# Performance work log

Measured on AMD Instinct MI355X. Metric: run time of the kernel, lower is better.

## Reference

```python
import jax, jax.numpy as jnp
import numpy as np

B, H, W, D = 8, 64, 64, 256   # batch, grid rows, grid cols, q_size==c_size
N = 1024                      # number of query/alignment points
R_WIN, C_WIN = 1, 2           # hardcoded window half-sizes from the module


def setup_inputs() -> dict:
    key = jax.random.key(0)
    k1, k2, k3, k4 = jax.random.split(key, 4)
    q = jax.random.normal(k1, (B, H, W, D), jnp.float32)
    c_t = jax.random.normal(k2, (B, N, D), jnp.float32)
    # float positions inside the grid: row in [0,H-1), col in [0,W-1)
    p_t = jax.random.uniform(k3, (B, N, 2), jnp.float32) * jnp.array([H - 1, W - 1], jnp.float32)
    W_a = jax.random.normal(k4, (D, D), jnp.float32) / np.sqrt(D)  # nn.Linear(q_size->c_size) weight [c,q]
    return {"q": q, "c_t": c_t, "p_t": p_t, "W_a": W_a}


def reference(q, c_t, p_t, W_a):
    Bq, Hh, Ww, Dd = q.shape
    rows, cols = Hh + 1, Ww + 1
    # ConstantPad2d((1,0,1,0), nan) on channels-first layout == pad top row & left col with NaN
    q_pad = jnp.pad(q.transpose(0, 3, 1, 2), ((0, 0), (0, 0), (1, 0), (1, 0)),
                    constant_values=jnp.nan)                      # [B,D,rows,cols]
    p0 = p_t[..., 0].astype(jnp.int32)
    p1 = p_t[..., 1].astype(jnp.int32)
    r = jnp.clip(p0[..., None] + jnp.arange(-R_WIN, R_WIN + 1) + 1, 0, rows) % rows  # [B,N,2R+1]
    c = jnp.clip(p1[..., None] + jnp.arange(-C_WIN, C_WIN + 1) + 1, 0, cols) % cols  # [B,N,2C+1]
    # flattened window indices, i (row offset) major, j (col offset) minor
    idx = (r[..., :, None] * cols + c[..., None, :]).reshape(Bq, r.shape[1], -1)     # [B,N,K]
    K = idx.shape[-1]
    q_flat = q_pad.reshape(Bq, Dd, rows * cols).transpose(0, 2, 1)                   # [B,rows*cols,D]
    qg = jnp.take_along_axis(q_flat, idx.reshape(Bq, -1, 1), axis=1)
    qg = qg.reshape(Bq, idx.shape[1], K, Dd)                                          # [B,N,K,D]
    nan_loc = jnp.isnan(qg[..., 0])                                                   # [B,N,K]
    qg = jnp.where(nan_loc[..., None], 0.0, qg)
    # Gaussian decay around the (float) predicted position
    rexp = jnp.exp(-2.0 * ((jnp.clip(r.astype(q.dtype) - 1, 0, None) - p_t[..., 0:1]) / R_WIN) ** 2)
    cexp = jnp.exp(-2.0 * ((jnp.clip(c.astype(q.dtype) - 1, 0, None) - p_t[..., 1:2]) / C_WIN) ** 2)
    expw = (rexp[..., :, None] * cexp[..., None, :]).reshape(Bq, r.shape[1], K)       # [B,N,K]
    # score: (W_a qg) . c_t per (b,n)
    Wa = jnp.einsum('bnkd,cd->bnkc', qg, W_a)
    a_t = jnp.einsum('bnkc,bnc->bnk', Wa, c_t)
    a_t = jnp.where(nan_loc, -jnp.inf, a_t)
    W_attn = jax.nn.softmax(a_t, axis=2) * expw
    return jnp.einsum('bnk,bnkd->bnd', W_attn, qg)                                    # [B,N,D]
```

## Files before the change

kernel.cpp:

```cpp
#include <hip/hip_runtime.h>
#include <math.h>

#define BATCH   8
#define HGRID   64
#define WGRID   64
#define DDIM    256
#define NPTS    1024
#define ROWS    65
#define COLS    65
#define KWIN    15
#define BN      (BATCH*NPTS)

#define PIDS_PER_BLK 16
#define THREADS      512
#define PR_PITCH     260
#define NPRE         4

typedef __attribute__((ext_vector_type(8))) short bf16x8;
typedef __attribute__((ext_vector_type(4))) float f32x4;

__global__ __launch_bounds__(THREADS, 4) void fused_local_attn(
        const float* __restrict__ q,
        const float* __restrict__ c_t,
        const float* __restrict__ p_t,
        const float* __restrict__ W,
        float* __restrict__ out) {

    __shared__ __align__(16) float Pr[PIDS_PER_BLK][PR_PITCH];

    const int t    = threadIdx.x;
    const int w    = t >> 6;
    const int lane = t & 63;
    const int l15  = lane & 15;
    const int g    = lane >> 4;
    const int bid  = blockIdx.x;
    const int wk   = (bid & 7) * 64 + (bid >> 3);
    const int pid0 = wk * PIDS_PER_BLK;
    const int dq   = w * 32;

    f32x4 acc0 = (f32x4)0.f;
    f32x4 acc1 = (f32x4)0.f;

    const float* ap  = &c_t[(size_t)(pid0 + l15) * DDIM + g * 8];
    const float* wp0 = &W[(size_t)(g * 8) * DDIM + dq + l15];
    const float* wp1 = wp0 + 16;

    #pragma unroll 2
    for (int kt = 0; kt < 8; ++kt) {
        const float4 a01 = *reinterpret_cast<const float4*>(ap + kt * 32);
        const float4 a23 = *reinterpret_cast<const float4*>(ap + kt * 32 + 4);
        const float af[8] = {a01.x, a01.y, a01.z, a01.w, a23.x, a23.y, a23.z, a23.w};
        union { bf16x8 v; unsigned u[4]; } AH, AL;
        #pragma unroll
        for (int i = 0; i < 4; ++i) {
            const unsigned u0 = __float_as_uint(af[2 * i]);
            const unsigned u1 = __float_as_uint(af[2 * i + 1]);
            AH.u[i] = __builtin_amdgcn_perm(u1, u0, 0x07060302u);
            const float l0 = af[2 * i]     - __uint_as_float(u0 & 0xFFFF0000u);
            const float l1 = af[2 * i + 1] - __uint_as_float(u1 & 0xFFFF0000u);
            AL.u[i] = __builtin_amdgcn_perm(__float_as_uint(l1), __float_as_uint(l0),
                                            0x07060302u);
        }

        #pragma unroll
        for (int df = 0; df < 2; ++df) {
            const float* wp = (df == 0) ? wp0 : wp1;
            float bf[8];
            #pragma unroll
            for (int i = 0; i < 8; ++i)
                bf[i] = wp[(size_t)(kt * 32 + i) * DDIM];
            union { bf16x8 v; unsigned u[4]; } BH, BL;
            #pragma unroll
            for (int i = 0; i < 4; ++i) {
                const unsigned u0 = __float_as_uint(bf[2 * i]);
                const unsigned u1 = __float_as_uint(bf[2 * i + 1]);
                BH.u[i] = __builtin_amdgcn_perm(u1, u0, 0x07060302u);
                const float l0 = bf[2 * i]     - __uint_as_float(u0 & 0xFFFF0000u);
                const float l1 = bf[2 * i + 1] - __uint_as_float(u1 & 0xFFFF0000u);
                BL.u[i] = __builtin_amdgcn_perm(__float_as_uint(l1), __float_as_uint(l0),
                                                0x07060302u);
            }
            f32x4 a = (df == 0) ? acc0 : acc1;
            a = __builtin_amdgcn_mfma_f32_16x16x32_bf16(AH.v, BH.v, a, 0, 0, 0);
            a = __builtin_amdgcn_mfma_f32_16x16x32_bf16(AH.v, BL.v, a, 0, 0, 0);
            a = __builtin_amdgcn_mfma_f32_16x16x32_bf16(AL.v, BH.v, a, 0, 0, 0);
            if (df == 0) acc0 = a; else acc1 = a;
        }
    }

    #pragma unroll
    for (int r = 0; r < 4; ++r) {
        Pr[g * 4 + r][dq +  0 + l15] = acc0[r];
        Pr[g * 4 + r][dq + 16 + l15] = acc1[r];
    }
    __syncthreads();

    const int pidA = pid0 + w * 2 + 0;
    const int pidB = pid0 + w * 2 + 1;
    const int b    = pidA >> 10;
    const float4 prA = *reinterpret_cast<const float4*>(&Pr[w * 2 + 0][lane * 4]);
    const float4 prB = *reinterpret_cast<const float4*>(&Pr[w * 2 + 1][lane * 4]);
    const float2 posA = *reinterpret_cast<const float2*>(&p_t[pidA * 2]);
    const float2 posB = *reinterpret_cast<const float2*>(&p_t[pidB * 2]);

    int rowA[3], colA[5];
    {
        const int p0 = (int)posA.x, p1 = (int)posA.y;
        #pragma unroll
        for (int i = 0; i < 3; ++i) {
            int rr = p0 + i;
            rr = rr > ROWS ? ROWS : rr;
            rowA[i] = (rr == ROWS) ? 0 : rr;
        }
        #pragma unroll
        for (int j = 0; j < 5; ++j) {
            int cc = p1 + j - 1;
            cc = cc < 0 ? 0 : (cc > COLS ? COLS : cc);
            colA[j] = (cc == COLS) ? 0 : cc;
        }
    }

    float4 qgA[KWIN];
    unsigned vmA = 0;
    #pragma unroll
    for (int k = 0; k < KWIN; ++k) {
        const int i = k / 5, j = k % 5;
        const int rr = rowA[i], cc = colA[j];
        if ((rr != 0) && (cc != 0)) vmA |= (1u << k);
        const int rrc = rr ? rr : 1;
        const int ccc = cc ? cc : 1;
        qgA[k] = *reinterpret_cast<const float4*>(
            &q[((size_t)((b * HGRID + rrc - 1) * WGRID + ccc - 1)) * DDIM + lane * 4]);
    }

    float reA[3], ceA[5];
    #pragma unroll
    for (int i = 0; i < 3; ++i) {
        const float rf = (float)(rowA[i] - 1 > 0 ? rowA[i] - 1 : 0);
        const float dr = rf - posA.x;
        reA[i] = __expf(-2.0f * dr * dr);
    }
    #pragma unroll
    for (int j = 0; j < 5; ++j) {
        const float cf = (float)(colA[j] - 1 > 0 ? colA[j] - 1 : 0);
        const float dc = (cf - posA.y) * 0.5f;
        ceA[j] = __expf(-2.0f * dc * dc);
    }

    __builtin_amdgcn_sched_barrier(0);

    int rowB[3], colB[5];
    {
        const int p0 = (int)posB.x, p1 = (int)posB.y;
        #pragma unroll
        for (int i = 0; i < 3; ++i) {
            int rr = p0 + i;
            rr = rr > ROWS ? ROWS : rr;
            rowB[i] = (rr == ROWS) ? 0 : rr;
        }
        #pragma unroll
        for (int j = 0; j < 5; ++j) {
            int cc = p1 + j - 1;
            cc = cc < 0 ? 0 : (cc > COLS ? COLS : cc);
            colB[j] = (cc == COLS) ? 0 : cc;
        }
    }
    unsigned vmB = 0;
    #pragma unroll
    for (int k = 0; k < KWIN; ++k) {
        const int i = k / 5, j = k % 5;
        if ((rowB[i] != 0) && (colB[j] != 0)) vmB |= (1u << k);
    }
    float4 qgBpre[NPRE];
    #pragma unroll
    for (int k = 0; k < NPRE; ++k) {
        const int i = k / 5, j = k % 5;
        const int rrc = rowB[i] ? rowB[i] : 1;
        const int ccc = colB[j] ? colB[j] : 1;
        qgBpre[k] = *reinterpret_cast<const float4*>(
            &q[((size_t)((b * HGRID + rrc - 1) * WGRID + ccc - 1)) * DDIM + lane * 4]);
    }

    asm volatile("s_waitcnt vmcnt(" "4" ")" ::: "memory");
    #pragma unroll
    for (int k = 0; k < KWIN; ++k)
        asm volatile("" : "+v"(qgA[k].x), "+v"(qgA[k].y), "+v"(qgA[k].z), "+v"(qgA[k].w));

    {
        float score[KWIN];
        #pragma unroll
        for (int k = 0; k < KWIN; ++k) {
            const float4 v = qgA[k];
            score[k] = fmaf(v.x, prA.x, fmaf(v.y, prA.y, fmaf(v.z, prA.z, v.w * prA.w)));
        }
        #pragma unroll
        for (int k = 0; k < KWIN; ++k) {
            float s = score[k];
            #pragma unroll
            for (int off = 32; off; off >>= 1) s += __shfl_xor(s, off, 64);
            score[k] = ((vmA >> k) & 1u) ? s : -INFINITY;
        }
        float mx = score[0];
        #pragma unroll
        for (int k = 1; k < KWIN; ++k) mx = fmaxf(mx, score[k]);
        float sum = 0.f;
        #pragma unroll
        for (int k = 0; k < KWIN; ++k) {
            const float e = __expf(score[k] - mx);
            score[k] = e;
            sum += e;
        }
        const float inv = 1.0f / sum;
        float ox = 0.f, oy = 0.f, oz = 0.f, ow = 0.f;
        #pragma unroll
        for (int k = 0; k < KWIN; ++k) {
            const int i = k / 5, j = k % 5;
            const float wk2 = score[k] * inv * reA[i] * ceA[j];
            ox = fmaf(wk2, qgA[k].x, ox);
            oy = fmaf(wk2, qgA[k].y, oy);
            oz = fmaf(wk2, qgA[k].z, oz);
            ow = fmaf(wk2, qgA[k].w, ow);
        }
        *reinterpret_cast<float4*>(&out[(size_t)pidA * DDIM + lane * 4]) =
            make_float4(ox, oy, oz, ow);
    }

    __builtin_amdgcn_sched_barrier(0);

    float4 qgBr[KWIN - NPRE];
    #pragma unroll
    for (int k = NPRE; k < KWIN; ++k) {
        const int i = k / 5, j = k % 5;
        const int rrc = rowB[i] ? rowB[i] : 1;
        const int ccc = colB[j] ? colB[j] : 1;
        qgBr[k - NPRE] = *reinterpret_cast<const float4*>(
            &q[((size_t)((b * HGRID + rrc - 1) * WGRID + ccc - 1)) * DDIM + lane * 4]);
    }

    float reB[3], ceB[5];
    #pragma unroll
    for (int i = 0; i < 3; ++i) {
        const float rf = (float)(rowB[i] - 1 > 0 ? rowB[i] - 1 : 0);
        const float dr = rf - posB.x;
        reB[i] = __expf(-2.0f * dr * dr);
    }
    #pragma unroll
    for (int j = 0; j < 5; ++j) {
        const float cf = (float)(colB[j] - 1 > 0 ? colB[j] - 1 : 0);
        const float dc = (cf - posB.y) * 0.5f;
        ceB[j] = __expf(-2.0f * dc * dc);
    }

    asm volatile("s_waitcnt vmcnt(0)" ::: "memory");
    #pragma unroll
    for (int k = 0; k < NPRE; ++k)
        asm volatile("" : "+v"(qgBpre[k].x), "+v"(qgBpre[k].y),
                          "+v"(qgBpre[k].z), "+v"(qgBpre[k].w));
    #pragma unroll
    for (int k = 0; k < KWIN - NPRE; ++k)
        asm volatile("" : "+v"(qgBr[k].x), "+v"(qgBr[k].y),
                          "+v"(qgBr[k].z), "+v"(qgBr[k].w));

    {
        float score[KWIN];
        #pragma unroll
        for (int k = 0; k < KWIN; ++k) {
            const float4 v = (k < NPRE) ? qgBpre[k] : qgBr[k - NPRE];
            score[k] = fmaf(v.x, prB.x, fmaf(v.y, prB.y, fmaf(v.z, prB.z, v.w * prB.w)));
        }
        #pragma unroll
        for (int k = 0; k < KWIN; ++k) {
            float s = score[k];
            #pragma unroll
            for (int off = 32; off; off >>= 1) s += __shfl_xor(s, off, 64);
            score[k] = ((vmB >> k) & 1u) ? s : -INFINITY;
        }
        float mx = score[0];
        #pragma unroll
        for (int k = 1; k < KWIN; ++k) mx = fmaxf(mx, score[k]);
        float sum = 0.f;
        #pragma unroll
        for (int k = 0; k < KWIN; ++k) {
            const float e = __expf(score[k] - mx);
            score[k] = e;
            sum += e;
        }
        const float inv = 1.0f / sum;
        float ox = 0.f, oy = 0.f, oz = 0.f, ow = 0.f;
        #pragma unroll
        for (int k = 0; k < KWIN; ++k) {
            const int i = k / 5, j = k % 5;
            const float wk2 = score[k] * inv * reB[i] * ceB[j];
            const float4 v = (k < NPRE) ? qgBpre[k] : qgBr[k - NPRE];
            ox = fmaf(wk2, v.x, ox);
            oy = fmaf(wk2, v.y, oy);
            oz = fmaf(wk2, v.z, oz);
            ow = fmaf(wk2, v.w, ow);
        }
        *reinterpret_cast<float4*>(&out[(size_t)pidB * DDIM + lane * 4]) =
            make_float4(ox, oy, oz, ow);
    }
}

extern "C" void kernel_launch(void* const* d_in, const int* in_sizes, int n_in,
                              void* d_out, int out_size, void* d_ws, size_t ws_size,
                              hipStream_t stream) {
    const float* q   = (const float*)d_in[0];
    const float* c_t = (const float*)d_in[1];
    const float* p_t = (const float*)d_in[2];
    const float* W_a = (const float*)d_in[3];
    float* out = (float*)d_out;

    fused_local_attn<<<BN / PIDS_PER_BLK, THREADS, 0, stream>>>(q, c_t, p_t, W_a, out);
}
```

Before: 38.39 us.

## Prefetch second point's window rows into LDS via direct global-to-LDS loads

```diff
diff --git a/kernel.cpp b/kernel.cpp
--- a/kernel.cpp
+++ b/kernel.cpp
@@ -14,10 +14,16 @@
 #define PIDS_PER_BLK 16
 #define THREADS      512
 #define PR_PITCH     260
-#define NPRE         4
+#define NLDSB        8
 
 typedef __attribute__((ext_vector_type(8))) short bf16x8;
 typedef __attribute__((ext_vector_type(4))) float f32x4;
+
+__device__ __forceinline__ void gload_lds16(const float* src, float* dst) {
+    __builtin_amdgcn_global_load_lds(
+        (const __attribute__((address_space(1))) unsigned int*)src,
+        (__attribute__((address_space(3))) unsigned int*)dst, 16, 0, 0);
+}
 
 __global__ __launch_bounds__(THREADS, 4) void fused_local_attn(
         const float* __restrict__ q,
@@ -26,7 +32,8 @@
         const float* __restrict__ W,
         float* __restrict__ out) {
 
-    __shared__ __align__(16) float Pr[PIDS_PER_BLK][PR_PITCH];
+    __shared__ __align__(16) float smem[NLDSB * DDIM * 8];
+    float (*Pr)[DDIM] = reinterpret_cast<float (*)[DDIM]>(smem);
 
     const int t    = threadIdx.x;
     const int w    = t >> 6;
@@ -37,6 +44,7 @@
     const int wk   = (bid & 7) * 64 + (bid >> 3);
     const int pid0 = wk * PIDS_PER_BLK;
     const int dq   = w * 32;
+    float* qsw = smem + w * (NLDSB * DDIM);
 
     f32x4 acc0 = (f32x4)0.f;
     f32x4 acc1 = (f32x4)0.f;
@@ -95,15 +103,17 @@
     }
     __syncthreads();
 
+    const float4 prA = *reinterpret_cast<const float4*>(&Pr[w * 2 + 0][lane * 4]);
+    const float4 prB = *reinterpret_cast<const float4*>(&Pr[w * 2 + 1][lane * 4]);
+    __syncthreads();
+
     const int pidA = pid0 + w * 2 + 0;
     const int pidB = pid0 + w * 2 + 1;
     const int b    = pidA >> 10;
-    const float4 prA = *reinterpret_cast<const float4*>(&Pr[w * 2 + 0][lane * 4]);
-    const float4 prB = *reinterpret_cast<const float4*>(&Pr[w * 2 + 1][lane * 4]);
     const float2 posA = *reinterpret_cast<const float2*>(&p_t[pidA * 2]);
     const float2 posB = *reinterpret_cast<const float2*>(&p_t[pidB * 2]);
 
-    int rowA[3], colA[5];
+    int rowA[3], colA[5], rowB[3], colB[5];
     {
         const int p0 = (int)posA.x, p1 = (int)posA.y;
         #pragma unroll
@@ -119,19 +129,54 @@
             colA[j] = (cc == COLS) ? 0 : cc;
         }
     }
-
-    float4 qgA[KWIN];
-    unsigned vmA = 0;
+    {
+        const int p0 = (int)posB.x, p1 = (int)posB.y;
+        #pragma unroll
+        for (int i = 0; i < 3; ++i) {
+            int rr = p0 + i;
+            rr = rr > ROWS ? ROWS : rr;
+            rowB[i] = (rr == ROWS) ? 0 : rr;
+        }
+        #pragma unroll
+        for (int j = 0; j < 5; ++j) {
+            int cc = p1 + j - 1;
+            cc = cc < 0 ? 0 : (cc > COLS ? COLS : cc);
+            colB[j] = (cc == COLS) ? 0 : cc;
+        }
+    }
+    unsigned vmA = 0, vmB = 0;
     #pragma unroll
     for (int k = 0; k < KWIN; ++k) {
         const int i = k / 5, j = k % 5;
-        const int rr = rowA[i], cc = colA[j];
-        if ((rr != 0) && (cc != 0)) vmA |= (1u << k);
-        const int rrc = rr ? rr : 1;
-        const int ccc = cc ? cc : 1;
-        qgA[k] = *reinterpret_cast<const float4*>(
-            &q[((size_t)((b * HGRID + rrc - 1) * WGRID + ccc - 1)) * DDIM + lane * 4]);
-    }
+        if ((rowA[i] != 0) && (colA[j] != 0)) vmA |= (1u << k);
+        if ((rowB[i] != 0) && (colB[j] != 0)) vmB |= (1u << k);
+    }
+
+    float4 qgA[KWIN];
+    #pragma unroll
+    for (int k = 0; k < KWIN; ++k) {
+        const int i = k / 5, j = k % 5;
+        float4 v = make_float4(0.f, 0.f, 0.f, 0.f);
+        if ((vmA >> k) & 1u) {
+            v = *reinterpret_cast<const float4*>(
+                &q[((size_t)((b * HGRID + rowA[i] - 1) * WGRID + colA[j] - 1)) * DDIM
+                   + lane * 4]);
+        }
+        qgA[k] = v;
+    }
+
+    __builtin_amdgcn_sched_barrier(0);
+
+    #pragma unroll
+    for (int k = 0; k < NLDSB; ++k) {
+        const int i = k / 5, j = k % 5;
+        const int rrc = rowB[i] ? rowB[i] : 1;
+        const int ccc = colB[j] ? colB[j] : 1;
+        gload_lds16(&q[((size_t)((b * HGRID + rrc - 1) * WGRID + ccc - 1)) * DDIM
+                       + lane * 4],
+                    &qsw[k * DDIM]);
+    }
+    __builtin_amdgcn_sched_barrier(0);
 
     float reA[3], ceA[5];
     #pragma unroll
@@ -147,41 +192,7 @@
         ceA[j] = __expf(-2.0f * dc * dc);
     }
 
-    __builtin_amdgcn_sched_barrier(0);
-
-    int rowB[3], colB[5];
-    {
-        const int p0 = (int)posB.x, p1 = (int)posB.y;
-        #pragma unroll
-        for (int i = 0; i < 3; ++i) {
-            int rr = p0 + i;
-            rr = rr > ROWS ? ROWS : rr;
-            rowB[i] = (rr == ROWS) ? 0 : rr;
-        }
-        #pragma unroll
-        for (int j = 0; j < 5; ++j) {
-            int cc = p1 + j - 1;
-            cc = cc < 0 ? 0 : (cc > COLS ? COLS : cc);
-            colB[j] = (cc == COLS) ? 0 : cc;
-        }
-    }
-    unsigned vmB = 0;
-    #pragma unroll
-    for (int k = 0; k < KWIN; ++k) {
-        const int i = k / 5, j = k % 5;
-        if ((rowB[i] != 0) && (colB[j] != 0)) vmB |= (1u << k);
-    }
-    float4 qgBpre[NPRE];
-    #pragma unroll
-    for (int k = 0; k < NPRE; ++k) {
-        const int i = k / 5, j = k % 5;
-        const int rrc = rowB[i] ? rowB[i] : 1;
-        const int ccc = colB[j] ? colB[j] : 1;
-        qgBpre[k] = *reinterpret_cast<const float4*>(
-            &q[((size_t)((b * HGRID + rrc - 1) * WGRID + ccc - 1)) * DDIM + lane * 4]);
-    }
-
-    asm volatile("s_waitcnt vmcnt(" "4" ")" ::: "memory");
+    asm volatile("s_waitcnt vmcnt(" "8" ")" ::: "memory");
     #pragma unroll
     for (int k = 0; k < KWIN; ++k)
         asm volatile("" : "+v"(qgA[k].x), "+v"(qgA[k].y), "+v"(qgA[k].z), "+v"(qgA[k].w));
@@ -227,14 +238,17 @@
 
     __builtin_amdgcn_sched_barrier(0);
 
-    float4 qgBr[KWIN - NPRE];
-    #pragma unroll
-    for (int k = NPRE; k < KWIN; ++k) {
+    float4 qgBr[KWIN - NLDSB];
+    #pragma unroll
+    for (int k = NLDSB; k < KWIN; ++k) {
         const int i = k / 5, j = k % 5;
-        const int rrc = rowB[i] ? rowB[i] : 1;
-        const int ccc = colB[j] ? colB[j] : 1;
-        qgBr[k - NPRE] = *reinterpret_cast<const float4*>(
-            &q[((size_t)((b * HGRID + rrc - 1) * WGRID + ccc - 1)) * DDIM + lane * 4]);
+        float4 v = make_float4(0.f, 0.f, 0.f, 0.f);
+        if ((vmB >> k) & 1u) {
+            v = *reinterpret_cast<const float4*>(
+                &q[((size_t)((b * HGRID + rowB[i] - 1) * WGRID + colB[j] - 1)) * DDIM
+                   + lane * 4]);
+        }
+        qgBr[k - NLDSB] = v;
     }
 
     float reB[3], ceB[5];
@@ -253,11 +267,7 @@
 
     asm volatile("s_waitcnt vmcnt(0)" ::: "memory");
     #pragma unroll
-    for (int k = 0; k < NPRE; ++k)
-        asm volatile("" : "+v"(qgBpre[k].x), "+v"(qgBpre[k].y),
-                          "+v"(qgBpre[k].z), "+v"(qgBpre[k].w));
-    #pragma unroll
-    for (int k = 0; k < KWIN - NPRE; ++k)
+    for (int k = 0; k < KWIN - NLDSB; ++k)
         asm volatile("" : "+v"(qgBr[k].x), "+v"(qgBr[k].y),
                           "+v"(qgBr[k].z), "+v"(qgBr[k].w));
 
@@ -265,7 +275,11 @@
         float score[KWIN];
         #pragma unroll
         for (int k = 0; k < KWIN; ++k) {
-            const float4 v = (k < NPRE) ? qgBpre[k] : qgBr[k - NPRE];
+            float4 v;
+            if (k < NLDSB)
+                v = *reinterpret_cast<const float4*>(&qsw[k * DDIM + lane * 4]);
+            else
+                v = qgBr[k - NLDSB];
             score[k] = fmaf(v.x, prB.x, fmaf(v.y, prB.y, fmaf(v.z, prB.z, v.w * prB.w)));
         }
         #pragma unroll
@@ -291,7 +305,11 @@
         for (int k = 0; k < KWIN; ++k) {
             const int i = k / 5, j = k % 5;
             const float wk2 = score[k] * inv * reB[i] * ceB[j];
-            const float4 v = (k < NPRE) ? qgBpre[k] : qgBr[k - NPRE];
+            float4 v;
+            if (k < NLDSB)
+                v = *reinterpret_cast<const float4*>(&qsw[k * DDIM + lane * 4]);
+            else
+                v = qgBr[k - NLDSB];
             ox = fmaf(wk2, v.x, ox);
             oy = fmaf(wk2, v.y, oy);
             oz = fmaf(wk2, v.z, oz);
```

New measurement: 33.80 us. 1.14x faster.
